# Kernel tuning notes

Measured on AMD Instinct MI355X. Metric: run time of the kernel, lower is better.

Reference implementation:

```python
import jax, jax.numpy as jnp
import numpy as np

B, N, DIM = 8, 1024, 256
NHEADS_GAT = 8
NHEADS_CA = 4
ALPHA = 0.2          # GAT LeakyReLU slope
NEG_GAT = -9.0e15    # mask value used by GraphAttentionLayer
NEG_CA = -1.0e9      # key mask value for cross-attention
THRESH = 0.97


def _ln(x, g, b, eps=1e-5):
    m = jnp.mean(x, axis=-1, keepdims=True)
    v = jnp.var(x, axis=-1, keepdims=True)
    return (x - m) / jnp.sqrt(v + eps) * g + b


def _leaky(z):
    return jnp.where(z >= 0, z, ALPHA * z)


def setup_inputs() -> dict:
    key = jax.random.key(0)
    ks = jax.random.split(key, 20)
    d = DIM
    xav = 1.414 * np.sqrt(2.0 / (2 * d))          # xavier gain 1.414 for GAT W
    xav_a = 1.414 * np.sqrt(2.0 / (2 * d + 1))    # for attention vectors a
    kaim = np.sqrt(2.0 / d)                       # kaiming for Linear layers
    inp = {
        "x": jax.random.normal(ks[0], (B, N, d), jnp.float32),
        "mask": jax.random.randint(ks[1], (B, N), 0, 2),
        "pos_emb": jax.random.normal(ks[2], (1, N, d), jnp.float32),
        # SimBlock (pos): bilinear-dot similarity; scaled so sigmoid>0.97 selects a real subset
        "sim_Wx": jax.random.normal(ks[3], (d, d), jnp.float32) * 0.7,
        "sim_Wq": jax.random.normal(ks[4], (d, d), jnp.float32) * 0.7,
        # AdjBlock: sigmoid gram-matrix adjacency
        "adj_W": jax.random.normal(ks[5], (d, d), jnp.float32) * (1.0 / np.sqrt(d)),
        # GAT: 8 heads (nfeat=dim -> nhid=dim, concat) + out layer (8*dim -> dim)
        "gat_W": jax.random.normal(ks[6], (NHEADS_GAT, d, d), jnp.float32) * xav,
        "gat_a1": jax.random.normal(ks[7], (NHEADS_GAT, d), jnp.float32) * xav_a,
        "gat_a2": jax.random.normal(ks[8], (NHEADS_GAT, d), jnp.float32) * xav_a,
        "gat_Wo": jax.random.normal(ks[9], (NHEADS_GAT * d, d), jnp.float32) * 1.414 * np.sqrt(2.0 / (NHEADS_GAT * d + d)),
        "gat_ao1": jax.random.normal(ks[10], (d,), jnp.float32) * xav_a,
        "gat_ao2": jax.random.normal(ks[11], (d,), jnp.float32) * xav_a,
        # LayerNorms 3/4 (only ones used in forward)
        "ln3_g": jnp.ones((d,), jnp.float32), "ln3_b": jnp.zeros((d,), jnp.float32),
        "ln4_g": jnp.ones((d,), jnp.float32), "ln4_b": jnp.zeros((d,), jnp.float32),
        # CrossAttention (4 heads, no qkv bias; proj bias init 0 -> omitted)
        "ca_Wq": jax.random.normal(ks[12], (d, d), jnp.float32) * kaim,
        "ca_Wk": jax.random.normal(ks[13], (d, d), jnp.float32) * kaim,
        "ca_Wv": jax.random.normal(ks[14], (d, d), jnp.float32) * kaim,
        "ca_Wp": jax.random.normal(ks[15], (d, d), jnp.float32) * kaim,
        "gamma": jax.random.normal(ks[16], (1, 1, d), jnp.float32),
    }
    return inp


def _gat(feat, connect, gat_W, gat_a1, gat_a2, gat_Wo, gat_ao1, gat_ao2):
    # feat: [N, d]; connect: [N, N] bool adjacency restricted to selected nodes
    Wh = jnp.einsum('nd,hde->hne', feat, gat_W)                      # [H, N, d]
    e = _leaky(jnp.einsum('hne,he->hn', Wh, gat_a1)[:, :, None]
               + jnp.einsum('hne,he->hn', Wh, gat_a2)[:, None, :])   # [H, N, N]
    attn = jax.nn.softmax(jnp.where(connect[None], e, NEG_GAT), axis=-1)
    h = jax.nn.elu(jnp.einsum('hnm,hme->hne', attn, Wh))             # [H, N, d]
    cat = jnp.transpose(h, (1, 0, 2)).reshape(feat.shape[0], -1)     # [N, H*d]
    Who = cat @ gat_Wo                                               # [N, d]
    eo = _leaky((Who @ gat_ao1)[:, None] + (Who @ gat_ao2)[None, :])
    attn_o = jax.nn.softmax(jnp.where(connect, eo, NEG_GAT), axis=-1)
    return jax.nn.elu(attn_o @ Who)                                  # [N, d]


def reference(x, mask, pos_emb, sim_Wx, sim_Wq, adj_W,
              gat_W, gat_a1, gat_a2, gat_Wo, gat_ao1, gat_ao2,
              ln3_g, ln3_b, ln4_g, ln4_b,
              ca_Wq, ca_Wk, ca_Wv, ca_Wp, gamma):
    d = x.shape[-1]
    inv_sqrt_d = 1.0 / jnp.sqrt(jnp.float32(d))
    # mean_query: masked mean over positive tokens
    pm = (mask == 1).astype(x.dtype)[..., None]                      # [B, N, 1]
    pos_query = (x * pm).sum(1) / jnp.maximum(pm.sum(1), 1.0)        # [B, d]
    # SimBlock + sigmoid -> per-token positive similarity
    pos_sim = jax.nn.sigmoid(
        jnp.einsum('bnd,bd->bn', x @ sim_Wx, pos_query @ sim_Wq) * inv_sqrt_d)
    sel = pos_sim > THRESH                                           # [B, N] bool

    dh = d // NHEADS_CA
    scale = 1.0 / jnp.sqrt(jnp.float32(dh))
    pe0 = pos_emb[0]                                                 # [N, d]

    def per_sample(feat, sel_i):
        # AdjBlock on full node set; restrict to selected x selected (equals
        # computing it on the gathered subset since it is pairwise)
        fa = feat @ adj_W
        adj = jax.nn.sigmoid((fa @ fa.T) * inv_sqrt_d)
        connect = (adj > 0.5) & sel_i[:, None] & sel_i[None, :]
        gout = _gat(feat, connect, gat_W, gat_a1, gat_a2, gat_Wo, gat_ao1, gat_ao2)
        q_full = jnp.where(sel_i[:, None], gout + pe0, 0.0)          # zero non-selected
        # CrossAttention(norm3(feat) -> queries, norm4(query nodes) -> keys/values)
        qx = _ln(feat, ln3_g, ln3_b)
        kv = _ln(q_full, ln4_g, ln4_b)
        q = (qx @ ca_Wq).reshape(-1, NHEADS_CA, dh)
        k = (kv @ ca_Wk).reshape(-1, NHEADS_CA, dh)
        v = (kv @ ca_Wv).reshape(-1, NHEADS_CA, dh)
        logits = jnp.einsum('nhd,mhd->hnm', q, k) * scale
        logits = jnp.where(sel_i[None, None, :], logits, NEG_CA)
        a = jax.nn.softmax(logits, axis=-1)
        o = jnp.einsum('hnm,mhd->nhd', a, v).reshape(-1, d) @ ca_Wp
        return feat + gamma[0, 0] * o

    x_out = jax.vmap(per_sample)(x, sel)
    return x_out, pos_sim
```

## Files before the change

kernel.cpp:

```cpp
#include <hip/hip_runtime.h>
#include <hip/hip_bf16.h>


#define BB 8
#define NN 1024
#define DD 256
#define HG 8
#define HC 4
#define BN (BB*NN)

typedef unsigned short u16;
typedef unsigned int u32;
typedef unsigned char u8;
typedef __attribute__((ext_vector_type(8))) short s8v;
typedef __attribute__((ext_vector_type(4))) float f4v;
#define MFMA(a,b,c) __builtin_amdgcn_mfma_f32_16x16x32_bf16((a),(b),(c),0,0,0)

__device__ __forceinline__ u16 f2b(float x){
  union{ float f; unsigned u; } a; a.f = x;
  unsigned r = a.u + 0x7fff + ((a.u>>16)&1);
  return (u16)(r>>16);
}
__device__ __forceinline__ float b2f(u16 b){ return __uint_as_float(((unsigned)b)<<16); }
__device__ __forceinline__ float4 ld4bf(const u16* p){
  uint2 u = *(const uint2*)p;
  float4 r;
  r.x=__uint_as_float(u.x<<16); r.y=__uint_as_float(u.x&0xffff0000u);
  r.z=__uint_as_float(u.y<<16); r.w=__uint_as_float(u.y&0xffff0000u);
  return r;
}
__device__ __forceinline__ void load8(const float* p, float* v){
  float4 a=*(const float4*)p, b=*(const float4*)(p+4);
  v[0]=a.x;v[1]=a.y;v[2]=a.z;v[3]=a.w;v[4]=b.x;v[5]=b.y;v[6]=b.z;v[7]=b.w;
}
__device__ __forceinline__ float wredsum(float v){
  #pragma unroll
  for(int o=32;o>0;o>>=1) v += __shfl_xor(v,o);
  return v;
}
__device__ __forceinline__ float wredmax(float v){
  #pragma unroll
  for(int o=32;o>0;o>>=1) v = fmaxf(v,__shfl_xor(v,o));
  return v;
}
__device__ __forceinline__ float eluf(float x){ return x>0.f ? x : __expf(x)-1.f; }
__device__ __forceinline__ float leakyf(float z){ return z>=0.f ? z : 0.2f*z; }
__device__ __forceinline__ float exp0(float a){ return __expf(fminf(a, 0.f)); }
__device__ __forceinline__ float flushf(float v){ return (fabsf(v) < 1.0e30f) ? v : 0.f; }
__device__ __forceinline__ u32 pk2(float lo, float hi){
  u32 r;
  asm("v_cvt_pk_bf16_f32 %0, %1, %2" : "=v"(r) : "v"(lo), "v"(hi));
  return r;
}

__device__ __forceinline__ size_t packIdx(int col, int row){
  int kk = row & 1023;
  return ((((size_t)(col>>4))*8 + (row>>10))*32 + (kk>>5))*512
       + (size_t)(((((kk>>3)&3)*16) + (col&15))*8 + (kk&7));
}

__device__ __forceinline__ size_t gpK(int row, int k, int KK){
  return (size_t)(row>>4)*((size_t)16*KK) + (size_t)(k>>5)*512
       + (size_t)(((((k>>3)&3)*16) + (row&15))*8 + (k&7));
}

__global__ __launch_bounds__(256) void k_split(const float* __restrict__ X, u16* __restrict__ H, u16* __restrict__ Lo){
  size_t i = ((size_t)blockIdx.x*256 + threadIdx.x)*8;
  float v[8]; load8(X+i, v);
  u16 hh[8], ll[8];
  #pragma unroll
  for (int j=0;j<8;j++){ hh[j]=f2b(v[j]); ll[j]=f2b(v[j]-b2f(hh[j])); }
  int row = (int)(i>>8), col = (int)(i&255);
  size_t off = gpK(row, col, 256);
  *(uint4*)(H+off)=*(uint4*)&hh[0];
  *(uint4*)(Lo+off)=*(uint4*)&ll[0];
}

__global__ __launch_bounds__(256) void k_transpose(const float* __restrict__ S, u16* __restrict__ D,
                                                   int R, int sliceElems, int pkKK){
  __shared__ float tl[64][65];
  const float* src = S + (size_t)blockIdx.z*sliceElems;
  u16* dst = D + (size_t)blockIdx.z*sliceElems;
  int C = gridDim.x*64;
  int bx=blockIdx.x*64, by=blockIdx.y*64;
  int tid=threadIdx.x, r=tid>>2, c0=(tid&3)*16;
  #pragma unroll
  for (int i=0;i<16;i+=4){
    float4 v = *(const float4*)(src + (size_t)(by+r)*C + bx + c0 + i);
    tl[r][c0+i]=v.x; tl[r][c0+i+1]=v.y; tl[r][c0+i+2]=v.z; tl[r][c0+i+3]=v.w;
  }
  __syncthreads();
  u16 tmp[16];
  #pragma unroll
  for (int i=0;i<16;i++) tmp[i] = f2b(tl[c0+i][r]);
  if (pkKK){
    *(uint4*)(dst + gpK(bx+r, by+c0,     pkKK)) = *(uint4*)&tmp[0];
    *(uint4*)(dst + gpK(bx+r, by+c0+8,   pkKK)) = *(uint4*)&tmp[8];
  } else {
    *(uint4*)(dst + (size_t)(bx+r)*R + by + c0)     = *(uint4*)&tmp[0];
    *(uint4*)(dst + (size_t)(bx+r)*R + by + c0 + 8) = *(uint4*)&tmp[8];
  }
}

__global__ __launch_bounds__(256) void k_transpose4(const float* __restrict__ Sa, const float* __restrict__ Sb,
    const float* __restrict__ Sc, const float* __restrict__ Sd, u16* __restrict__ D){
  __shared__ float tl[64][65];
  const float* src = blockIdx.z==0 ? Sa : blockIdx.z==1 ? Sb : blockIdx.z==2 ? Sc : Sd;
  u16* dst = D + (size_t)blockIdx.z*65536;
  int bx=blockIdx.x*64, by=blockIdx.y*64;
  int tid=threadIdx.x, r=tid>>2, c0=(tid&3)*16;
  #pragma unroll
  for (int i=0;i<16;i+=4){
    float4 v = *(const float4*)(src + (size_t)(by+r)*256 + bx + c0 + i);
    tl[r][c0+i]=v.x; tl[r][c0+i+1]=v.y; tl[r][c0+i+2]=v.z; tl[r][c0+i+3]=v.w;
  }
  __syncthreads();
  u16 tmp[16];
  #pragma unroll
  for (int i=0;i<16;i++) tmp[i] = f2b(tl[c0+i][r]);
  *(uint4*)(dst + gpK(bx+r, by+c0,   256)) = *(uint4*)&tmp[0];
  *(uint4*)(dst + gpK(bx+r, by+c0+8, 256)) = *(uint4*)&tmp[8];
}

__global__ __launch_bounds__(256) void k_transp_split(const float* __restrict__ S, u16* __restrict__ DH, u16* __restrict__ DL){
  __shared__ float tl[64][65];
  int bx=blockIdx.x*64, by=blockIdx.y*64;
  int tid=threadIdx.x, r=tid>>2, c0=(tid&3)*16;
  #pragma unroll
  for (int i=0;i<16;i+=4){
    float4 v = *(const float4*)(S + (size_t)(by+r)*256 + bx + c0 + i);
    tl[r][c0+i]=v.x; tl[r][c0+i+1]=v.y; tl[r][c0+i+2]=v.z; tl[r][c0+i+3]=v.w;
  }
  __syncthreads();
  u16 th[16], tll[16];
  #pragma unroll
  for (int i=0;i<16;i++){
    float v = tl[c0+i][r];
    th[i]=f2b(v); tll[i]=f2b(v - b2f(th[i]));
  }
  size_t o0 = gpK(bx+r, by+c0,   256);
  size_t o1 = gpK(bx+r, by+c0+8, 256);
  *(uint4*)(DH + o0) = *(uint4*)&th[0];
  *(uint4*)(DH + o1) = *(uint4*)&th[8];
  *(uint4*)(DL + o0) = *(uint4*)&tll[0];
  *(uint4*)(DL + o1) = *(uint4*)&tll[8];
}

__global__ __launch_bounds__(256) void k_posq(const float* __restrict__ x, const int* __restrict__ mask,
                                              float* __restrict__ pq, float* __restrict__ cnt){
  int b = blockIdx.x, chunk = blockIdx.y;
  int d = threadIdx.x;
  int n0 = chunk*64;
  float acc = 0.f; float c = 0.f;
  for (int i=0;i<64;i++){
    int n = n0+i;
    if (mask[b*NN+n]==1){ acc += x[((size_t)(b*NN+n))*DD + d]; c += 1.f; }
  }
  atomicAdd(&pq[b*DD+d], acc);
  if (d==0) atomicAdd(&cnt[b], c);
}

__global__ __launch_bounds__(256) void k_sq(const float* __restrict__ pq, const float* __restrict__ cnt,
                                            const float* __restrict__ Wq, float* __restrict__ sq){
  int b = blockIdx.x, e = threadIdx.x;
  float inv = 1.f / fmaxf(cnt[b], 1.f);
  float acc=0.f;
  for (int d0=0; d0<DD; d0++) acc += (pq[b*DD+d0]*inv) * Wq[d0*DD+e];
  sq[b*DD+e] = acc;
}

__global__ __launch_bounds__(256) void k_simsel2(const float* __restrict__ pdot,
                                                 float* __restrict__ simOut, u8* __restrict__ sel8){
  int r = blockIdx.x*256 + threadIdx.x;
  float s = pdot[r] * 0.0625f;
  float sim = 1.f/(1.f+expf(-s));
  simOut[r] = sim;
  sel8[r] = (sim > 0.97f) ? 1 : 0;
}

template<int EPI, int APK, int BPK, int UNR=1>
__global__ __launch_bounds__(256) void k_mgemm(const u16* __restrict__ A, const u16* __restrict__ BT,
    int KK, int ldB, int kOff, float* __restrict__ C, const float* __restrict__ Xres,
    const float* __restrict__ gamma, u16* __restrict__ O, u16* __restrict__ Pk,
    const float* __restrict__ A1, const float* __restrict__ A2,
    float* __restrict__ s1g, float* __restrict__ s2g){
  int tid=threadIdx.x, w=tid>>6, lane=tid&63, L=lane&15, q=lane>>4;
  int OC = gridDim.x<<6;
  int colBase=blockIdx.x<<6, rowBase=blockIdx.y<<6;
  const u16* ap;
  if constexpr (APK) ap = A + (size_t)((rowBase>>4)+w)*((size_t)16*KK) + (size_t)lane*8;
  else               ap = A + (size_t)(rowBase + w*16 + L)*KK + q*8;
  const u16* bp[4];
  #pragma unroll
  for (int t=0;t<4;t++){
    if constexpr (BPK) bp[t] = BT + (size_t)((colBase>>4)+t)*((size_t)16*ldB) + (size_t)(kOff>>5)*512 + (size_t)lane*8;
    else               bp[t] = BT + (size_t)(colBase + t*16 + L)*ldB + q*8 + kOff;
  }
  f4v z4={0.f,0.f,0.f,0.f};
  f4v acc[4]={z4,z4,z4,z4};
  int nk = KK>>5;
  for (int kc0=0;kc0<nk;kc0+=UNR){
    s8v a0[UNR], bt[UNR][4];
    #pragma unroll
    for (int u=0;u<UNR;u++){
      int kc = kc0 + u;
      if constexpr (APK) a0[u] = *(const s8v*)(ap + (size_t)kc*512);
      else               a0[u] = *(const s8v*)(ap + kc*32);
      #pragma unroll
      for (int t=0;t<4;t++){
        if constexpr (BPK) bt[u][t] = *(const s8v*)(bp[t] + (size_t)kc*512);
        else               bt[u][t] = *(const s8v*)(bp[t] + kc*32);
      }
    }
    #pragma unroll
    for (int u=0;u<UNR;u++)
      #pragma unroll
      for (int t=0;t<4;t++)
        acc[t]=MFMA(a0[u],bt[u][t],acc[t]);
  }
  if constexpr (EPI<=3){
    #pragma unroll
    for (int t=0;t<4;t++){
      int col = colBase + t*16 + L;
      #pragma unroll
      for (int reg=0;reg<4;reg++){
        int row = rowBase + w*16 + q*4 + reg;
        size_t off = (size_t)row*OC + col;
        float v = acc[t][reg];
        if constexpr (EPI==0){ C[off] = v; }
        else if constexpr (EPI==1){ C[off] += v; }
        else if constexpr (EPI==2){ C[off] = flushf(Xres[off] + gamma[col]*v); }
        else { O[off] = f2b(v); }
      }
    }
  } else {
    float s1p[4]={0.f,0.f,0.f,0.f}, s2p[4]={0.f,0.f,0.f,0.f};
    #pragma unroll
    for (int t=0;t<4;t++){
      int col = colBase + t*16 + L;
      float a1v = A1[col], a2v = A2[col];
      #pragma unroll
      for (int reg=0;reg<4;reg++){
        float v = acc[t][reg];
        s1p[reg] += v*a1v;
        s2p[reg] += v*a2v;
      }
    }
    #pragma unroll
    for (int off=1;off<16;off<<=1)
      #pragma unroll
      for (int reg=0;reg<4;reg++){
        s1p[reg] += __shfl_xor(s1p[reg],off);
        s2p[reg] += __shfl_xor(s2p[reg],off);
      }
    if (L==0){
      int sOff = (EPI==7) ? (colBase>>8)*BN : 0;
      #pragma unroll
      for (int reg=0;reg<4;reg++){
        int row = rowBase + w*16 + q*4 + reg;
        atomicAdd(&s1g[sOff+row], s1p[reg]);
        atomicAdd(&s2g[sOff+row], s2p[reg]);
      }
    }
    int pq_ = q&1;
    int m0 = rowBase + w*16 + (q>>1)*8;
    #pragma unroll
    for (int tp=0;tp<2;tp++){
      f4v accA = acc[2*tp], accB = acc[2*tp+1];
      f4v mine   = pq_ ? accB : accA;
      f4v theirs = pq_ ? accA : accB;
      u32 k0 = pk2(mine[0],  mine[1]);
      u32 k1 = pk2(mine[2],  mine[3]);
      u32 s0 = pk2(theirs[0],theirs[1]);
      u32 s1 = pk2(theirs[2],theirs[3]);
      u32 r0 = (u32)__shfl_xor((int)s0,16);
      u32 r1 = (u32)__shfl_xor((int)s1,16);
      uint4 val = pq_==0 ? make_uint4(k0,k1,r0,r1) : make_uint4(r0,r1,k0,k1);
      int t = 2*tp + pq_;
      int col = colBase + t*16 + L;
      *(uint4*)(Pk + packIdx(col, m0)) = val;
    }
  }
}

__global__ __launch_bounds__(256) void k_mgemm3(const u16* __restrict__ Aq, const u16* __restrict__ Akv,
    const u16* __restrict__ BT0, u16* __restrict__ O0){
  int tid=threadIdx.x, w=tid>>6, lane=tid&63, L=lane&15, q=lane>>4;
  const u16* A = blockIdx.z==0 ? Aq : Akv;
  const u16* BT = BT0 + (size_t)blockIdx.z*65536;
  u16* O = O0 + (size_t)blockIdx.z*2097152;
  int colBase=blockIdx.x<<6, rowBase=blockIdx.y<<6;
  const u16* ap = A + (size_t)((rowBase>>4)+w)*4096 + (size_t)lane*8;
  f4v z4={0.f,0.f,0.f,0.f};
  f4v acc[4]={z4,z4,z4,z4};
  #pragma unroll
  for (int kc=0;kc<8;kc++){
    s8v a0 = *(const s8v*)(ap + kc*512);
    #pragma unroll
    for (int t=0;t<4;t++){
      s8v bt = *(const s8v*)(BT + (size_t)((colBase>>4)+t)*4096 + (size_t)kc*512 + (size_t)lane*8);
      acc[t]=MFMA(a0,bt,acc[t]);
    }
  }
  #pragma unroll
  for (int t=0;t<4;t++){
    int col = colBase + t*16 + L;
    #pragma unroll
    for (int reg=0;reg<4;reg++){
      int row = rowBase + w*16 + q*4 + reg;
      O[(size_t)row*256 + col] = f2b(acc[t][reg]);
    }
  }
}

template<int EPI>
__global__ __launch_bounds__(256) void k_msgemm(const u16* __restrict__ Ah, const u16* __restrict__ Al,
    const u16* __restrict__ Bh, const u16* __restrict__ Bl,
    float* __restrict__ C, u16* __restrict__ Oh, u16* __restrict__ Ol,
    const float* __restrict__ sq, float* __restrict__ pdot){
  int tid=threadIdx.x, w=tid>>6, lane=tid&63, L=lane&15, q=lane>>4;
  int colBase=blockIdx.x<<6, rowBase=blockIdx.y<<6;
  const u16* ahp = Ah + (size_t)((rowBase>>4)+w)*4096 + (size_t)lane*8;
  const u16* alp = Al + (size_t)((rowBase>>4)+w)*4096 + (size_t)lane*8;
  f4v z4={0.f,0.f,0.f,0.f};
  f4v acc[4]={z4,z4,z4,z4};
  #pragma unroll
  for (int kc=0;kc<8;kc++){
    s8v ah=*(const s8v*)(ahp + kc*512), al=*(const s8v*)(alp + kc*512);
    #pragma unroll
    for (int t=0;t<4;t++){
      size_t boff = (size_t)((colBase>>4)+t)*4096 + (size_t)kc*512 + (size_t)lane*8;
      s8v bh=*(const s8v*)(Bh + boff);
      s8v bl=*(const s8v*)(Bl + boff);
      acc[t]=MFMA(ah,bh,acc[t]);
      acc[t]=MFMA(ah,bl,acc[t]);
      acc[t]=MFMA(al,bh,acc[t]);
    }
  }
  if constexpr (EPI==5){
    int b = rowBase>>10;
    float pp[4]={0.f,0.f,0.f,0.f};
    #pragma unroll
    for (int t=0;t<4;t++){
      int col = colBase + t*16 + L;
      float qv = sq[b*256 + col];
      #pragma unroll
      for (int reg=0;reg<4;reg++) pp[reg] += acc[t][reg]*qv;
    }
    #pragma unroll
    for (int off=1;off<16;off<<=1)
      #pragma unroll
      for (int reg=0;reg<4;reg++) pp[reg] += __shfl_xor(pp[reg],off);
    if (L==0){
      #pragma unroll
      for (int reg=0;reg<4;reg++){
        int row = rowBase + w*16 + q*4 + reg;
        atomicAdd(&pdot[row], pp[reg]);
      }
    }
  } else {
    #pragma unroll
    for (int t=0;t<4;t++){
      int col = colBase + t*16 + L;
      #pragma unroll
      for (int reg=0;reg<4;reg++){
        int row = rowBase + w*16 + q*4 + reg;
        float v = acc[t][reg];
        if constexpr (EPI==0){ C[(size_t)row*256 + col] = v; }
        else {
          size_t off = gpK(row, col, 256);
          u16 h = f2b(v); Oh[off]=h; Ol[off]=f2b(v - b2f(h));
        }
      }
    }
  }
}

__global__ __launch_bounds__(256) void k_mconnect2(const u16* __restrict__ fahP, const u16* __restrict__ falP,
    const u8* __restrict__ sel8, u32* __restrict__ conn){
  __shared__ u8 sg[64][64];
  __shared__ u8 selI[64], selJ[64];
  int tid=threadIdx.x, w=tid>>6, lane=tid&63, L=lane&15, q=lane>>4;
  int b=blockIdx.z;
  int p=blockIdx.x;
  int i = (int)((sqrtf(8.f*p+1.f)-1.f)*0.5f);
  while ((i+1)*(i+2)/2 <= p) i++;
  while (i*(i+1)/2 > p) i--;
  int j = p - i*(i+1)/2;
  if (tid < 64)        selI[tid]     = sel8[b*NN + i*64 + tid];
  else if (tid < 128)  selJ[tid-64]  = sel8[b*NN + j*64 + (tid-64)];
  const u16* ah0 = fahP + ((size_t)(b*64 + i*4 + w))*4096 + (size_t)lane*8;
  const u16* al0 = falP + ((size_t)(b*64 + i*4 + w))*4096 + (size_t)lane*8;
  const u16* bh0 = fahP + ((size_t)(b*64 + j*4))*4096 + (size_t)lane*8;
  const u16* bl0 = falP + ((size_t)(b*64 + j*4))*4096 + (size_t)lane*8;
  f4v z4={0.f,0.f,0.f,0.f};
  f4v acc[4]={z4,z4,z4,z4};
  #pragma unroll
  for (int kc=0;kc<8;kc++){
    s8v ah = *(const s8v*)(ah0 + kc*512);
    s8v al = *(const s8v*)(al0 + kc*512);
    #pragma unroll
    for (int t=0;t<4;t++){
      s8v bh = *(const s8v*)(bh0 + (size_t)t*4096 + kc*512);
      s8v bl = *(const s8v*)(bl0 + (size_t)t*4096 + kc*512);
      acc[t]=MFMA(ah,bh,acc[t]);
      acc[t]=MFMA(ah,bl,acc[t]);
      acc[t]=MFMA(al,bh,acc[t]);
    }
  }
  #pragma unroll
  for (int t=0;t<4;t++)
    #pragma unroll
    for (int reg=0;reg<4;reg++)
      sg[w*16 + q*4 + reg][t*16 + L] = acc[t][reg] > 0.f;
  __syncthreads();
  int row=(tid&127)>>1, ww=tid&1;
  if (tid<128){
    u32 word=0;
    if (selI[row]){
      #pragma unroll 8
      for (int jj=0;jj<32;jj++)
        if (sg[row][ww*32+jj] && selJ[ww*32+jj]) word |= (1u<<jj);
    }
    conn[((size_t)b*NN + i*64+row)*32 + j*2 + ww] = word;
  } else if (i != j){
    u32 word=0;
    if (selJ[row]){
      #pragma unroll 8
      for (int jj=0;jj<32;jj++)
        if (sg[ww*32+jj][row] && selI[ww*32+jj]) word |= (1u<<jj);
    }
    conn[((size_t)b*NN + j*64+row)*32 + i*2 + ww] = word;
  }
}

__global__ __launch_bounds__(256) void k_rowmax(const float* __restrict__ s2a,
    const u32* __restrict__ conn, float* __restrict__ M2a){
  int h = blockIdx.y;
  int r = blockIdx.x*4 + (threadIdx.x>>6);
  int lane = threadIdx.x&63;
  int b = r>>10;
  const float* s2p = s2a + h*BN + b*NN;
  float mx = -3.0e38f;
  #pragma unroll
  for (int t=0;t<16;t++){
    int m = lane + t*64;
    u32 wd = conn[(size_t)r*32 + (m>>5)];
    if ((wd>>(m&31))&1u) mx = fmaxf(mx, s2p[m]);
  }
  mx = wredmax(mx);
  if (lane==0) M2a[h*BN+r] = mx;
}

template<int CT, bool SWZ, int PKO>
__global__ __launch_bounds__(256,4) void k_mattn5(const float* __restrict__ s1a, const float* __restrict__ s2a,
    const float* __restrict__ M2a, const u32* __restrict__ conn,
    const u16* __restrict__ P, int headMul, u16* __restrict__ Out, int oStride){
  __shared__ __align__(16) u16 Pb[2][4][512];
  __shared__ float Srow[64];
  int tid=threadIdx.x, w=tid>>6, lane=tid&63, L=lane&15, q=lane>>4;
  int h, rowBlk;
  if constexpr (SWZ){ h = blockIdx.y & 7; rowBlk = (blockIdx.y>>3) + (blockIdx.z<<4); }
  else             { h = blockIdx.z;     rowBlk = blockIdx.y; }
  int rowBase = rowBlk*64;
  int hOff = h*headMul, sOff = h*BN;
  int b = rowBase>>10;
  size_t bOff = (size_t)b*NN;
  int r = rowBase + w*16 + L;
  float s1v = s1a[sOff+r];
  float rmv = leakyf(s1v + M2a[sOff+r]);
  const float* s2p = s2a + sOff + bOff;
  const u32* cp = conn + (size_t)r*32;
  int tile0 = blockIdx.x*(4*CT) + w*CT;
  const u16* vp = P + (size_t)((hOff>>4) + tile0)*131072 + (size_t)b*16384 + (size_t)lane*8;
  f4v z4={0.f,0.f,0.f,0.f};
  f4v acc[4][CT];
  #pragma unroll
  for (int g=0;g<4;g++)
    #pragma unroll
    for (int t=0;t<CT;t++) acc[g][t]=z4;
  float sumP = 0.f;
  for (int k0=0;k0<NN;k0+=32){
    int cur=(k0>>5)&1;
    u32 cw = cp[k0>>5];
    s8v vf[CT];
    {
      const u16* vk = vp + (size_t)(k0>>5)*512;
      #pragma unroll
      for (int t=0;t<CT;t++) vf[t] = *(const s8v*)(vk + (size_t)t*131072);
    }
    float4 sA = *(const float4*)(s2p + k0 + q*8);
    float4 sB = *(const float4*)(s2p + k0 + q*8 + 4);
    float s2v[8] = {sA.x,sA.y,sA.z,sA.w,sB.x,sB.y,sB.z,sB.w};
    float p[8];
    #pragma unroll
    for (int j=0;j<8;j++){
      float z = s1v + s2v[j];
      float ev = fmaxf(z, 0.2f*z);
      ev = ((cw>>(q*8+j))&1u) ? ev : -9.0e15f;
      p[j] = __expf(fminf(ev - rmv, 0.f));
      sumP += p[j];
    }
    union{ s8v v; u32 u[4]; } pk;
    #pragma unroll
    for (int jj=0;jj<4;jj++)
      pk.u[jj] = pk2(p[2*jj], p[2*jj+1]);
    *(s8v*)&Pb[cur][w][lane*8] = pk.v;
    __syncthreads();
    s8v pa[4];
    #pragma unroll
    for (int g=0;g<4;g++) pa[g] = *(const s8v*)&Pb[cur][g][lane*8];
    #pragma unroll
    for (int t=0;t<CT;t++)
      #pragma unroll
      for (int g=0;g<4;g++) acc[g][t] = MFMA(pa[g], vf[t], acc[g][t]);
  }
  sumP += __shfl_xor(sumP,16);
  sumP += __shfl_xor(sumP,32);
  if (lane<16) Srow[w*16+lane] = sumP;
  __syncthreads();
  #pragma unroll
  for (int g=0;g<4;g++){
    float4 sv = *(const float4*)&Srow[g*16 + q*4];
    float rsi[4] = {1.f/sv.x, 1.f/sv.y, 1.f/sv.z, 1.f/sv.w};
    #pragma unroll
    for (int t=0;t<CT;t++){
      int col = hOff + (tile0+t)*16 + L;
      #pragma unroll
      for (int reg=0;reg<4;reg++){
        int row = rowBase + g*16 + q*4 + reg;
        float ov = eluf(acc[g][t][reg]*rsi[reg]);
        if constexpr (PKO) Out[gpK(row, col, PKO)] = f2b(ov);
        else               Out[(size_t)row*oStride + col] = f2b(ov);
      }
    }
  }
}

__global__ __launch_bounds__(256) void k_ln_x(const float* __restrict__ x, const float* __restrict__ g,
                                              const float* __restrict__ bb, u16* __restrict__ out){
  int r = blockIdx.x*4 + (threadIdx.x>>6);
  int lane=threadIdx.x&63;
  float4 v = *(const float4*)(x + (size_t)r*DD + lane*4);
  float s = v.x+v.y+v.z+v.w;
  float s2 = v.x*v.x+v.y*v.y+v.z*v.z+v.w*v.w;
  s = wredsum(s); s2 = wredsum(s2);
  float mean = s*(1.f/256.f);
  float var = s2*(1.f/256.f) - mean*mean;
  float rstd = rsqrtf(var + 1e-5f);
  float4 gv = *(const float4*)(g+lane*4), bv = *(const float4*)(bb+lane*4);
  u16 t[4];
  t[0]=f2b((v.x-mean)*rstd*gv.x+bv.x); t[1]=f2b((v.y-mean)*rstd*gv.y+bv.y);
  t[2]=f2b((v.z-mean)*rstd*gv.z+bv.z); t[3]=f2b((v.w-mean)*rstd*gv.w+bv.w);
  *(uint2*)(out + gpK(r, lane*4, 256)) = *(uint2*)&t[0];
}

__global__ __launch_bounds__(256) void k_ln_kv(const u16* __restrict__ gout, const float* __restrict__ pe,
    const u8* __restrict__ sel8, const float* __restrict__ g, const float* __restrict__ bb,
    u16* __restrict__ out){
  int r = blockIdx.x*4 + (threadIdx.x>>6);
  int lane=threadIdx.x&63;
  int n = r & 1023;
  float4 v = make_float4(0.f,0.f,0.f,0.f);
  if (sel8[r]){
    float4 gv = ld4bf(gout + (size_t)r*DD + lane*4);
    float4 pv = *(const float4*)(pe + (size_t)n*DD + lane*4);
    v = make_float4(gv.x+pv.x, gv.y+pv.y, gv.z+pv.z, gv.w+pv.w);
  }
  float s = v.x+v.y+v.z+v.w;
  float s2 = v.x*v.x+v.y*v.y+v.z*v.z+v.w*v.w;
  s = wredsum(s); s2 = wredsum(s2);
  float mean = s*(1.f/256.f);
  float var = s2*(1.f/256.f) - mean*mean;
  float rstd = rsqrtf(var + 1e-5f);
  float4 gv = *(const float4*)(g+lane*4), bv = *(const float4*)(bb+lane*4);
  u16 t[4];
  t[0]=f2b((v.x-mean)*rstd*gv.x+bv.x); t[1]=f2b((v.y-mean)*rstd*gv.y+bv.y);
  t[2]=f2b((v.z-mean)*rstd*gv.z+bv.z); t[3]=f2b((v.w-mean)*rstd*gv.w+bv.w);
  *(uint2*)(out + gpK(r, lane*4, 256)) = *(uint2*)&t[0];
}

__global__ __launch_bounds__(256) void k_mca_av2(const u16* __restrict__ q, const u16* __restrict__ k,
    const u16* __restrict__ v, const u8* __restrict__ sel8, u16* __restrict__ O){
  __shared__ __align__(16) u16 Qls[64][72];
  __shared__ __align__(16) u16 KP[64][72];
  __shared__ __align__(16) u16 Vt[64][72];
  int tid=threadIdx.x;
  int w = tid>>6, lane = tid&63, L = lane&15, qd = lane>>4;
  int b=blockIdx.z, h=blockIdx.y, rowBase=blockIdx.x*64;
  size_t bOff = (size_t)b*NN;
  {
    int r=tid>>2, c0=(tid&3)*16;
    size_t base = (bOff + rowBase + r)*(size_t)DD + h*64 + c0;
    *(uint4*)&Qls[r][c0]   = *(const uint4*)(q + base);
    *(uint4*)&Qls[r][c0+8] = *(const uint4*)(q + base + 8);
  }
  float rm[4], sp[4];
  #pragma unroll
  for (int reg=0;reg<4;reg++){ rm[reg] = -3.0e38f; sp[reg] = 0.f; }
  f4v zero = {0.f,0.f,0.f,0.f};
  f4v acc[4] = {zero,zero,zero,zero};
  int svm = tid&63, svd0 = (tid>>6)*16;
  for (int m0=0;m0<NN;m0+=64){
    __syncthreads();
    {
      int r=tid>>2, c0=(tid&3)*16;
      size_t base = (bOff + m0 + r)*(size_t)DD + h*64 + c0;
      *(uint4*)&KP[r][c0]   = *(const uint4*)(k + base);
      *(uint4*)&KP[r][c0+8] = *(const uint4*)(k + base + 8);
      size_t vb_ = (bOff + m0 + svm)*(size_t)DD + h*64 + svd0;
      uint4 u0 = *(const uint4*)(v + vb_);
      uint4 u1 = *(const uint4*)(v + vb_ + 8);
      u16 tmp[16];
      *(uint4*)&tmp[0]=u0; *(uint4*)&tmp[8]=u1;
      #pragma unroll
      for (int i=0;i<16;i++) Vt[svd0+i][svm] = tmp[i];
    }
    __syncthreads();
    f4v sa[4] = {zero,zero,zero,zero};
    #pragma unroll
    for (int kc=0;kc<64;kc+=32){
      s8v af = *(const s8v*)&Qls[w*16 + L][kc + qd*8];
      #pragma unroll
      for (int t=0;t<4;t++){
        s8v bfr = *(const s8v*)&KP[t*16 + L][kc + qd*8];
        sa[t] = MFMA(af, bfr, sa[t]);
      }
    }
    __syncthreads();
    float vals[4][4];
    float tmax[4];
    #pragma unroll
    for (int reg=0;reg<4;reg++) tmax[reg] = -3.0e38f;
    #pragma unroll
    for (int t=0;t<4;t++){
      int m = m0 + t*16 + L;
      bool sl = sel8[b*NN+m];
      #pragma unroll
      for (int reg=0;reg<4;reg++){
        float val = sl ? sa[t][reg]*0.125f : -1.0e9f;
        vals[t][reg] = val;
        tmax[reg] = fmaxf(tmax[reg], val);
      }
    }
    #pragma unroll
    for (int off=1;off<16;off<<=1)
      #pragma unroll
      for (int reg=0;reg<4;reg++) tmax[reg] = fmaxf(tmax[reg], __shfl_xor(tmax[reg],off));
    float sc[4];
    #pragma unroll
    for (int reg=0;reg<4;reg++){
      float nm = fmaxf(rm[reg], tmax[reg]);
      sc[reg] = exp0(rm[reg] - nm);
      rm[reg] = nm;
      sp[reg] *= sc[reg];
    }
    #pragma unroll
    for (int t=0;t<4;t++){
      #pragma unroll
      for (int reg=0;reg<4;reg++){
        float pv = exp0(vals[t][reg] - rm[reg]);
        sp[reg] += pv;
        KP[w*16 + qd*4 + reg][t*16 + L] = f2b(pv);
      }
    }
    #pragma unroll
    for (int t=0;t<4;t++)
      #pragma unroll
      for (int reg=0;reg<4;reg++) acc[t][reg] *= sc[reg];
    __syncthreads();
    #pragma unroll
    for (int mc=0;mc<64;mc+=32){
      s8v pf = *(const s8v*)&KP[w*16 + L][mc + qd*8];
      #pragma unroll
      for (int t=0;t<4;t++){
        s8v vf = *(const s8v*)&Vt[t*16 + L][mc + qd*8];
        acc[t] = MFMA(pf, vf, acc[t]);
      }
    }
  }
  #pragma unroll
  for (int off=1;off<16;off<<=1)
    #pragma unroll
    for (int reg=0;reg<4;reg++) sp[reg] += __shfl_xor(sp[reg],off);
  float ri[4];
  #pragma unroll
  for (int reg=0;reg<4;reg++) ri[reg] = 1.f/sp[reg];
  #pragma unroll
  for (int t=0;t<4;t++){
    int col = h*64 + t*16 + L;
    #pragma unroll
    for (int reg=0;reg<4;reg++){
      int row = (int)bOff + rowBase + w*16 + qd*4 + reg;
      O[gpK(row, col, 256)] = f2b(acc[t][reg]*ri[reg]);
    }
  }
}

extern "C" void kernel_launch(void* const* d_in, const int* in_sizes, int n_in,
                              void* d_out, int out_size, void* d_ws, size_t ws_size,
                              hipStream_t stream) {
  (void)in_sizes; (void)n_in; (void)out_size;
  const float* x      = (const float*)d_in[0];
  const int*   mask   = (const int*  )d_in[1];
  const float* pe     = (const float*)d_in[2];
  const float* sim_Wx = (const float*)d_in[3];
  const float* sim_Wq = (const float*)d_in[4];
  const float* adj_W  = (const float*)d_in[5];
  const float* gat_W  = (const float*)d_in[6];
  const float* gat_a1 = (const float*)d_in[7];
  const float* gat_a2 = (const float*)d_in[8];
  const float* gat_Wo = (const float*)d_in[9];
  const float* gat_ao1= (const float*)d_in[10];
  const float* gat_ao2= (const float*)d_in[11];
  const float* ln3_g  = (const float*)d_in[12];
  const float* ln3_b  = (const float*)d_in[13];
  const float* ln4_g  = (const float*)d_in[14];
  const float* ln4_b  = (const float*)d_in[15];
  const float* ca_Wq  = (const float*)d_in[16];
  const float* ca_Wk  = (const float*)d_in[17];
  const float* ca_Wv  = (const float*)d_in[18];
  const float* ca_Wp  = (const float*)d_in[19];
  const float* gamma  = (const float*)d_in[20];
  float* out    = (float*)d_out;
  float* simOut = out + (size_t)BN*DD;

  const size_t MB = 1024*1024;
  bool big = ws_size >= 98*MB;
  char* W = (char*)d_ws;
  float* pq   = (float*)W;
  float* cnt  = pq + 2048;
  float* sq   = cnt + 16;
  float* s1a  = (float*)(W + 64*1024);
  float* s2a  = (float*)(W + 320*1024);
  float* M2a  = (float*)(W + 576*1024);
  float* pdot = (float*)(W + 1216*1024);
  u8*    sel8 = (u8*)(W + 1400*1024);
  u32*   conn = (u32*)(W + 2*MB);
  u16*   WT0  = (u16*)(W + 3*MB);
  u16*   WoT  = (u16*)(W + 4*MB);
  u16*   WQT  = (u16*)(W + 5*MB);
  u16*   WPT  = WQT + 3*65536;
  u16*   sWxh = (u16*)(W + 5*MB + 512*1024);
  u16*   sWxl = sWxh + 65536;
  u16*   aWh  = sWxl + 65536;
  u16*   aWl  = aWh + 65536;
  u16*   xh   = (u16*)(W + 6*MB);
  u16*   xl   = (u16*)(W + 10*MB);
  float* S0   = (float*)(W + 14*MB);
  u16*   fah  = (u16*)(W + 22*MB);
  u16*   fal  = (u16*)(W + 26*MB);
  u16*   T2   = (u16*)(W + 30*MB);

  k_split<<<BN*DD/2048,256,0,stream>>>(x, xh, xl);
  k_transpose<<<dim3(4,4,HG),256,0,stream>>>(gat_W, WT0, 256, 65536, 256);
  k_transpose<<<dim3(4,32,1),256,0,stream>>>(gat_Wo, WoT, 2048, 0, 2048);
  k_transpose4<<<dim3(4,4,4),256,0,stream>>>(ca_Wq, ca_Wk, ca_Wv, ca_Wp, WQT);
  k_transp_split<<<dim3(4,4,1),256,0,stream>>>(sim_Wx, sWxh, sWxl);
  k_transp_split<<<dim3(4,4,1),256,0,stream>>>(adj_W, aWh, aWl);

  hipMemsetAsync(pq, 0, (2048+16)*sizeof(float), stream);
  hipMemsetAsync(pdot, 0, BN*sizeof(float), stream);
  k_posq<<<dim3(BB,16),256,0,stream>>>(x, mask, pq, cnt);
  k_sq<<<BB,256,0,stream>>>(pq, cnt, sim_Wq, sq);
  k_msgemm<5><<<dim3(4,128),256,0,stream>>>(xh, xl, sWxh, sWxl, nullptr, nullptr, nullptr, sq, pdot);
  k_simsel2<<<BN/256,256,0,stream>>>(pdot, simOut, sel8);
  k_msgemm<4><<<dim3(4,128),256,0,stream>>>(xh, xl, aWh, aWl, nullptr, fah, fal, nullptr, nullptr);
  k_mconnect2<<<dim3(136,1,BB),256,0,stream>>>(fah, fal, sel8, conn);

  if (big){
    u16* WhP   = (u16*)(W + 66*MB);
    u16* htcat = (u16*)(W + 34*MB);
    u16* S0P   = (u16*)(W + 22*MB);
    u16* qx = (u16*)(W + 34*MB);
    u16* kv = (u16*)(W + 38*MB);
    u16* qb = (u16*)(W + 42*MB);
    u16* vb = (u16*)(W + 50*MB);
    u16* Ob = (u16*)(W + 54*MB);

    hipMemsetAsync(s1a, 0, 512*1024, stream);
    k_mgemm<7,1,1><<<dim3(32,128),256,0,stream>>>(xh, WT0, 256, 256, 0, nullptr, nullptr, nullptr, nullptr,
                                                  WhP, gat_a1, gat_a2, s1a, s2a);
    k_rowmax<<<dim3(BN/4,HG),256,0,stream>>>(s2a, conn, M2a);
    k_mattn5<4,true,2048><<<dim3(1,128,HG),256,0,stream>>>(s1a, s2a, M2a, conn, WhP, 256, htcat, 2048);
    hipMemsetAsync(s1a, 0, BN*sizeof(float), stream);
    hipMemsetAsync(s2a, 0, BN*sizeof(float), stream);
    k_mgemm<8,1,1,4><<<dim3(4,128),256,0,stream>>>(htcat, WoT, 2048, 2048, 0, nullptr, nullptr, nullptr, nullptr,
                                                   S0P, gat_ao1, gat_ao2, s1a, s2a);
    k_rowmax<<<dim3(BN/4,1),256,0,stream>>>(s2a, conn, M2a);
    k_mattn5<1,false,0><<<dim3(4,128,1),256,0,stream>>>(s1a, s2a, M2a, conn, S0P, 0, T2, 256);

    k_ln_x<<<BN/4,256,0,stream>>>(x, ln3_g, ln3_b, qx);
    k_ln_kv<<<BN/4,256,0,stream>>>(T2, pe, sel8, ln4_g, ln4_b, kv);
    k_mgemm3<<<dim3(4,128,3),256,0,stream>>>(qx, kv, WQT, qb);
    k_mca_av2<<<dim3(16,HC,BB),256,0,stream>>>(qb, qb + 2097152, vb, sel8, Ob);
    k_mgemm<2,1,1,4><<<dim3(4,128),256,0,stream>>>(Ob, WPT, 256, 256, 0, out, x, gamma, nullptr, nullptr,
                                                   nullptr, nullptr, nullptr, nullptr);
  } else {
    u16* T0 = fah;
    u16* T1 = fal;
    u16* S0b = (u16*)S0;
    hipMemsetAsync(s1a, 0, 512*1024, stream);
    for (int h=0;h<HG;h++){
      hipMemsetAsync(s1a, 0, BN*sizeof(float), stream);
      hipMemsetAsync(s2a, 0, BN*sizeof(float), stream);
      k_mgemm<8,1,1><<<dim3(4,128),256,0,stream>>>(xh, WT0 + (size_t)h*65536, 256, 256, 0,
                                                   nullptr, nullptr, nullptr, nullptr, T0,
                                                   gat_a1 + h*DD, gat_a2 + h*DD, s1a, s2a);
      k_rowmax<<<dim3(BN/4,1),256,0,stream>>>(s2a, conn, M2a);
      k_mattn5<1,false,0><<<dim3(4,128,1),256,0,stream>>>(s1a, s2a, M2a, conn, T0, 0, T1, 256);
      k_mgemm<1,0,1><<<dim3(4,128),256,0,stream>>>(T1, WoT, 256, 2048, h*256, S0, nullptr, nullptr, nullptr, nullptr,
                                                   nullptr, nullptr, nullptr, nullptr);
    }
    hipMemsetAsync(s1a, 0, BN*sizeof(float), stream);
    hipMemsetAsync(s2a, 0, BN*sizeof(float), stream);
    k_mattn5<1,false,0><<<dim3(4,128,1),256,0,stream>>>(s1a, s2a, M2a, conn, (u16*)S0, 0, T2, 256);
    k_ln_x<<<BN/4,256,0,stream>>>(x, ln3_g, ln3_b, T1);
    k_ln_kv<<<BN/4,256,0,stream>>>(T2, pe, sel8, ln4_g, ln4_b, T0);
    k_mgemm3<<<dim3(4,128,3),256,0,stream>>>(T1, T0, WQT, S0b);
    k_mca_av2<<<dim3(16,HC,BB),256,0,stream>>>(S0b, S0b + 2097152, S0b + 4194304, sel8, T0);
    k_mgemm<2,1,1><<<dim3(4,128),256,0,stream>>>(T0, WPT, 256, 256, 0, out, x, gamma, nullptr, nullptr,
                                                 nullptr, nullptr, nullptr, nullptr);
  }
}
```

Before: 468.0 us.

## Store Q/K/V in MFMA-fragment layout and drop LDS staging in cross-attention

The QKV projection kernel now writes Q and K in the packed fragment layout (gpK) and V in a transposed packed layout (packIdx). The cross-attention kernel then loads MFMA operands straight from global memory into registers, with no shared-memory staging and no in-LDS transpose of V. Only a small per-wave P buffer stays in LDS, and all block-wide barriers are gone. The cost is that every wave redundantly loads the same K/V fragments from global memory/L2, and there is no shared reuse across the four waves.

Measured after the change: 462.9 us. No clear change (-1.1%).

```diff
diff --git a/kernel.cpp b/kernel.cpp
--- a/kernel.cpp
+++ b/kernel.cpp
@@ -302,13 +302,16 @@
       acc[t]=MFMA(a0,bt,acc[t]);
     }
   }
+  bool isV = (blockIdx.z==2);
   #pragma unroll
   for (int t=0;t<4;t++){
     int col = colBase + t*16 + L;
     #pragma unroll
     for (int reg=0;reg<4;reg++){
       int row = rowBase + w*16 + q*4 + reg;
-      O[(size_t)row*256 + col] = f2b(acc[t][reg]);
+      u16 hv = f2b(acc[t][reg]);
+      if (isV) O[packIdx(col, row)] = hv;
+      else     O[gpK(row, col, 256)] = hv;
     }
   }
 }
@@ -580,54 +583,42 @@
   *(uint2*)(out + gpK(r, lane*4, 256)) = *(uint2*)&t[0];
 }
 
-__global__ __launch_bounds__(256) void k_mca_av2(const u16* __restrict__ q, const u16* __restrict__ k,
+__global__ __launch_bounds__(256) void k_mca_av3(const u16* __restrict__ q, const u16* __restrict__ k,
     const u16* __restrict__ v, const u8* __restrict__ sel8, u16* __restrict__ O){
-  __shared__ __align__(16) u16 Qls[64][72];
-  __shared__ __align__(16) u16 KP[64][72];
-  __shared__ __align__(16) u16 Vt[64][72];
+  __shared__ __align__(16) u16 Pw[4][16][72];
   int tid=threadIdx.x;
   int w = tid>>6, lane = tid&63, L = lane&15, qd = lane>>4;
   int b=blockIdx.z, h=blockIdx.y, rowBase=blockIdx.x*64;
   size_t bOff = (size_t)b*NN;
-  {
-    int r=tid>>2, c0=(tid&3)*16;
-    size_t base = (bOff + rowBase + r)*(size_t)DD + h*64 + c0;
-    *(uint4*)&Qls[r][c0]   = *(const uint4*)(q + base);
-    *(uint4*)&Qls[r][c0+8] = *(const uint4*)(q + base + 8);
-  }
+  const u16* qbase = q + (size_t)((bOff + rowBase + w*16)>>4)*4096 + (size_t)lane*8;
+  s8v af0 = *(const s8v*)(qbase + (size_t)(h*2+0)*512);
+  s8v af1 = *(const s8v*)(qbase + (size_t)(h*2+1)*512);
   float rm[4], sp[4];
   #pragma unroll
   for (int reg=0;reg<4;reg++){ rm[reg] = -3.0e38f; sp[reg] = 0.f; }
   f4v zero = {0.f,0.f,0.f,0.f};
   f4v acc[4] = {zero,zero,zero,zero};
-  int svm = tid&63, svd0 = (tid>>6)*16;
   for (int m0=0;m0<NN;m0+=64){
-    __syncthreads();
-    {
-      int r=tid>>2, c0=(tid&3)*16;
-      size_t base = (bOff + m0 + r)*(size_t)DD + h*64 + c0;
-      *(uint4*)&KP[r][c0]   = *(const uint4*)(k + base);
-      *(uint4*)&KP[r][c0+8] = *(const uint4*)(k + base + 8);
-      size_t vb_ = (bOff + m0 + svm)*(size_t)DD + h*64 + svd0;
-      uint4 u0 = *(const uint4*)(v + vb_);
-      uint4 u1 = *(const uint4*)(v + vb_ + 8);
-      u16 tmp[16];
-      *(uint4*)&tmp[0]=u0; *(uint4*)&tmp[8]=u1;
-      #pragma unroll
-      for (int i=0;i<16;i++) Vt[svd0+i][svm] = tmp[i];
-    }
-    __syncthreads();
+    s8v bt[4][2];
+    #pragma unroll
+    for (int t=0;t<4;t++){
+      const u16* kb = k + (size_t)((bOff + m0 + t*16)>>4)*4096 + (size_t)lane*8;
+      bt[t][0] = *(const s8v*)(kb + (size_t)(h*2+0)*512);
+      bt[t][1] = *(const s8v*)(kb + (size_t)(h*2+1)*512);
+    }
+    s8v vf[4][2];
+    #pragma unroll
+    for (int t=0;t<4;t++){
+      const u16* vb = v + (size_t)(((h*4+t)*8 + b)*32 + (m0>>5))*512 + (size_t)lane*8;
+      vf[t][0] = *(const s8v*)vb;
+      vf[t][1] = *(const s8v*)(vb + 512);
+    }
     f4v sa[4] = {zero,zero,zero,zero};
     #pragma unroll
-    for (int kc=0;kc<64;kc+=32){
-      s8v af = *(const s8v*)&Qls[w*16 + L][kc + qd*8];
-      #pragma unroll
-      for (int t=0;t<4;t++){
-        s8v bfr = *(const s8v*)&KP[t*16 + L][kc + qd*8];
-        sa[t] = MFMA(af, bfr, sa[t]);
-      }
-    }
-    __syncthreads();
+    for (int t=0;t<4;t++){
+      sa[t] = MFMA(af0, bt[t][0], sa[t]);
+      sa[t] = MFMA(af1, bt[t][1], sa[t]);
+    }
     float vals[4][4];
     float tmax[4];
     #pragma unroll
@@ -661,22 +652,19 @@
       for (int reg=0;reg<4;reg++){
         float pv = exp0(vals[t][reg] - rm[reg]);
         sp[reg] += pv;
-        KP[w*16 + qd*4 + reg][t*16 + L] = f2b(pv);
+        Pw[w][qd*4 + reg][t*16 + L] = f2b(pv);
       }
     }
     #pragma unroll
     for (int t=0;t<4;t++)
       #pragma unroll
       for (int reg=0;reg<4;reg++) acc[t][reg] *= sc[reg];
-    __syncthreads();
-    #pragma unroll
-    for (int mc=0;mc<64;mc+=32){
-      s8v pf = *(const s8v*)&KP[w*16 + L][mc + qd*8];
-      #pragma unroll
-      for (int t=0;t<4;t++){
-        s8v vf = *(const s8v*)&Vt[t*16 + L][mc + qd*8];
-        acc[t] = MFMA(pf, vf, acc[t]);
-      }
+    #pragma unroll
+    for (int mc2=0;mc2<2;mc2++){
+      s8v pf = *(const s8v*)&Pw[w][L][mc2*32 + qd*8];
+      #pragma unroll
+      for (int t=0;t<4;t++)
+        acc[t] = MFMA(pf, vf[t][mc2], acc[t]);
     }
   }
   #pragma unroll
@@ -793,7 +781,7 @@
     k_ln_x<<<BN/4,256,0,stream>>>(x, ln3_g, ln3_b, qx);
     k_ln_kv<<<BN/4,256,0,stream>>>(T2, pe, sel8, ln4_g, ln4_b, kv);
     k_mgemm3<<<dim3(4,128,3),256,0,stream>>>(qx, kv, WQT, qb);
-    k_mca_av2<<<dim3(16,HC,BB),256,0,stream>>>(qb, qb + 2097152, vb, sel8, Ob);
+    k_mca_av3<<<dim3(16,HC,BB),256,0,stream>>>(qb, qb + 2097152, vb, sel8, Ob);
     k_mgemm<2,1,1,4><<<dim3(4,128),256,0,stream>>>(Ob, WPT, 256, 256, 0, out, x, gamma, nullptr, nullptr,
                                                    nullptr, nullptr, nullptr, nullptr);
   } else {
@@ -818,7 +806,7 @@
     k_ln_x<<<BN/4,256,0,stream>>>(x, ln3_g, ln3_b, T1);
     k_ln_kv<<<BN/4,256,0,stream>>>(T2, pe, sel8, ln4_g, ln4_b, T0);
     k_mgemm3<<<dim3(4,128,3),256,0,stream>>>(T1, T0, WQT, S0b);
-    k_mca_av2<<<dim3(16,HC,BB),256,0,stream>>>(S0b, S0b + 2097152, S0b + 4194304, sel8, T0);
+    k_mca_av3<<<dim3(16,HC,BB),256,0,stream>>>(S0b, S0b + 2097152, S0b + 4194304, sel8, T0);
     k_mgemm<2,1,1><<<dim3(4,128),256,0,stream>>>(T0, WPT, 256, 256, 0, out, x, gamma, nullptr, nullptr,
                                                  nullptr, nullptr, nullptr, nullptr);
   }
```
